# Optimization experiments

Measured on AMD Instinct MI355X. Metric: run time of the kernel, lower is better.

The kernel has to match this reference:

```python
import jax, jax.numpy as jnp
import numpy as np

N = 50000   # nodes
E = 800000  # edges
G = 64      # graphs
NEG_SLOPE = 0.2  # PyG GATConv leaky_relu slope


def gat_conv(x, edge_index, edge_attr, W, att_src, att_dst, We, att_edge, bias, num_nodes):
    # PyG GATConv, add_self_loops=False, concat=True, eval (no dropout)
    H, C = att_src.shape
    h = (x @ W).reshape(-1, H, C)                      # [N,H,C]
    a_src = (h * att_src).sum(-1)                      # [N,H]
    a_dst = (h * att_dst).sum(-1)                      # [N,H]
    src, dst = edge_index[0], edge_index[1]
    e = (edge_attr @ We).reshape(-1, H, C)             # [E,H,C]
    a_edge = (e * att_edge).sum(-1)                    # [E,H]
    alpha = a_src[src] + a_dst[dst] + a_edge           # [E,H]
    alpha = jax.nn.leaky_relu(alpha, NEG_SLOPE)
    # segment softmax over incoming edges of each dst node
    amax = jax.ops.segment_max(alpha, dst, num_segments=num_nodes)
    amax = jnp.where(jnp.isfinite(amax), amax, 0.0)
    ex = jnp.exp(alpha - amax[dst])
    denom = jax.ops.segment_sum(ex, dst, num_segments=num_nodes)
    att = ex / (denom[dst] + 1e-16)                    # [E,H]
    msg = h[src] * att[..., None]                      # [E,H,C]
    out = jax.ops.segment_sum(msg, dst, num_segments=num_nodes)
    return out.reshape(num_nodes, H * C) + bias


def setup_inputs() -> dict:
    key = jax.random.key(0)
    ks = jax.random.split(key, 20)
    s = 0.1
    inp = {
        "x": jax.random.normal(ks[0], (N, 128), jnp.float32),
        "edge_index": jax.random.randint(ks[1], (2, E), 0, N, dtype=jnp.int32),
        "edge_attr": jax.random.normal(ks[2], (E, 1), jnp.float32),
        "batch": jnp.sort(jax.random.randint(ks[3], (N,), 0, G, dtype=jnp.int32)),
        # layer 1: 128 -> 4 heads x 32
        "W1": jax.random.normal(ks[4], (128, 128), jnp.float32) * s,
        "as1": jax.random.normal(ks[5], (4, 32), jnp.float32) * s,
        "ad1": jax.random.normal(ks[6], (4, 32), jnp.float32) * s,
        "We1": jax.random.normal(ks[7], (1, 128), jnp.float32) * s,
        "ae1": jax.random.normal(ks[8], (4, 32), jnp.float32) * s,
        "b1": jnp.zeros((128,), jnp.float32),
        # layer 2: 128 -> 1 head x 64
        "W2": jax.random.normal(ks[9], (128, 64), jnp.float32) * s,
        "as2": jax.random.normal(ks[10], (1, 64), jnp.float32) * s,
        "ad2": jax.random.normal(ks[11], (1, 64), jnp.float32) * s,
        "We2": jax.random.normal(ks[12], (1, 64), jnp.float32) * s,
        "ae2": jax.random.normal(ks[13], (1, 64), jnp.float32) * s,
        "b2": jnp.zeros((64,), jnp.float32),
        # prediction head
        "Wp": jax.random.normal(ks[14], (64, 1), jnp.float32) * s,
        "bp": jnp.zeros((1,), jnp.float32),
    }
    return inp


def reference(x, edge_index, edge_attr, batch, W1, as1, ad1, We1, ae1, b1,
              W2, as2, ad2, We2, ae2, b2, Wp, bp):
    h = gat_conv(x, edge_index, edge_attr, W1, as1, ad1, We1, ae1, b1, N)
    h = jax.nn.relu(h)  # dropout p=0.0, eval mode
    h = gat_conv(h, edge_index, edge_attr, W2, as2, ad2, We2, ae2, b2, N)
    # per-graph mean pooling (vectorized replacement of the python loop)
    counts = jax.ops.segment_sum(jnp.ones((N,), h.dtype), batch, num_segments=G)
    sums = jax.ops.segment_sum(h, batch, num_segments=G)   # [G,64]
    mean = sums / counts[:, None]
    out = mean @ Wp + bp                                   # [G,1]
    return out.squeeze(-1)                                 # [G]
```

## Files before the change

kernel.cpp:

```cpp
#include <hip/hip_runtime.h>
#include <hip/hip_bf16.h>

typedef unsigned short u16;
typedef unsigned int u32;

#define MAXB 2048
#define POOL_MAXG 64

typedef __attribute__((ext_vector_type(8))) short bf16x8;
typedef __attribute__((ext_vector_type(4))) float f32x4;

__device__ __forceinline__ float bf2f(u16 u) { return __uint_as_float(((u32)u) << 16); }
__device__ __forceinline__ float bl(u32 u) { return __uint_as_float(u << 16); }
__device__ __forceinline__ float bh(u32 u) { return __uint_as_float(u & 0xffff0000u); }
__device__ __forceinline__ u16 f2bf(float f) {
    u32 u = __float_as_uint(f);
    u += 0x7fffu + ((u >> 16) & 1u);
    return (u16)(u >> 16);
}
__device__ __forceinline__ float lrelu(float x) { return x > 0.f ? x : 0.2f * x; }
__device__ __forceinline__ int clampi(int v, int lo, int hi) {
    return v < lo ? lo : (v > hi ? hi : v);
}
__device__ __forceinline__ float load1(const void* base, int idx, int f32) {
    return f32 ? ((const float*)base)[idx] : bf2f(((const u16*)base)[idx]);
}
__device__ __forceinline__ float cexpf(float a) {
    return __builtin_amdgcn_exp2f(fminf(a, 30.f) * 1.4426950408889634f);
}

__global__ void k_init(const u32* __restrict__ xw, int* __restrict__ flag,
                       int* __restrict__ bcnt, int B,
                       const void* We1, const void* ae1, const void* We2, const void* ae2,
                       const void* as1, const void* ad1, const void* as2, const void* ad2,
                       float* __restrict__ consts, float* __restrict__ pool, int psize) {
    __shared__ int sf;
    int t = threadIdx.x;
    for (int i = t; i < B; i += 256) bcnt[i] = 0;
    if (t < 64) {
        int cnt = 0;
        #pragma unroll
        for (int j = 0; j < 4; j++) {
            u32 w = xw[t * 4 + j];
            int e0 = (int)((w >> 7) & 0xffu);
            int e1 = (int)((w >> 23) & 0xffu);
            cnt += (e0 >= 0x60 && e0 <= 0x8f);
            cnt += (e1 >= 0x60 && e1 <= 0x8f);
        }
        #pragma unroll
        for (int off = 32; off > 0; off >>= 1) cnt += __shfl_xor(cnt, off);
        if (t == 0) { int v = (cnt < 480) ? 1 : 0; *flag = v; sf = v; }
    }
    __syncthreads();
    int f = sf;
    for (int i = t; i < psize; i += 256) pool[i] = 0.f;
    if (t < 4) {
        float s = 0.f;
        for (int c = 0; c < 32; c++) s += load1(We1, t * 32 + c, f) * load1(ae1, t * 32 + c, f);
        consts[t] = s;
    } else if (t == 4) {
        float s = 0.f;
        for (int c = 0; c < 64; c++) s += load1(We2, c, f) * load1(ae2, c, f);
        consts[4] = s;
    }
    if (t < 128) {
        consts[8 + t] = load1(as1, t, f);
        consts[136 + t] = load1(ad1, t, f);
    }
    if (t < 64) {
        consts[264 + t] = load1(as2, t, f);
        consts[328 + t] = load1(ad2, t, f);
    }
}

template <int NC>
__global__ __launch_bounds__(256, 2) void k_gemm_mfma(
    const void* __restrict__ X, const void* __restrict__ Wg,
    const int* __restrict__ flag, int fXovr, u16* __restrict__ Y,
    const float* __restrict__ consts, float* __restrict__ casrc,
    float* __restrict__ cadst, int nrows) {
    constexpr int NCT = NC / 16;
    __shared__ __align__(16) u16 Bf[2][NCT][4][64][8];

    const int f = *flag;
    const bool fX = (fXovr < 0) ? (f != 0) : (fXovr != 0);
    const bool fW = (f != 0);
    const int tid = threadIdx.x;
    const int wid = tid >> 6, lane = tid & 63;

    for (int idx = tid; idx < NCT * 4 * 64; idx += 256) {
        int l = idx & 63;
        int s = (idx >> 6) & 3;
        int t = idx >> 8;
        int col = t * 16 + (l & 15);
        int k0 = s * 32 + (l >> 4) * 8;
        u16 hi[8], lo[8];
        #pragma unroll
        for (int j = 0; j < 8; j++) {
            int k = k0 + j;
            int srow = (NC == 64) ? ((k & 1) * 64 + (k >> 1)) : k;
            float v = fW ? ((const float*)Wg)[srow * NC + col]
                         : bf2f(((const u16*)Wg)[srow * NC + col]);
            u16 h = f2bf(v);
            hi[j] = h;
            lo[j] = fW ? f2bf(v - bf2f(h)) : (u16)0;
        }
        uint4 hv, lv;
        hv.x = (u32)hi[0] | ((u32)hi[1] << 16);
        hv.y = (u32)hi[2] | ((u32)hi[3] << 16);
        hv.z = (u32)hi[4] | ((u32)hi[5] << 16);
        hv.w = (u32)hi[6] | ((u32)hi[7] << 16);
        lv.x = (u32)lo[0] | ((u32)lo[1] << 16);
        lv.y = (u32)lo[2] | ((u32)lo[3] << 16);
        lv.z = (u32)lo[4] | ((u32)lo[5] << 16);
        lv.w = (u32)lo[6] | ((u32)lo[7] << 16);
        *(uint4*)&Bf[0][t][s][l][0] = hv;
        *(uint4*)&Bf[1][t][s][l][0] = lv;
    }
    __syncthreads();

    const int tiles = (nrows + 63) >> 6;
    for (int tile = blockIdx.x; tile < tiles; tile += gridDim.x) {
        const int rowbase = tile * 64 + wid * 16;
        const int arow = rowbase + (lane & 15);
        const bool rv = arow < nrows;

        bf16x8 ahi[4], alo[4];
        #pragma unroll
        for (int s = 0; s < 4; s++) {
            int koff = s * 32 + (lane >> 4) * 8;
            u16 h[8], l8[8];
            #pragma unroll
            for (int j = 0; j < 8; j++) { h[j] = 0; l8[j] = 0; }
            if (rv) {
                if (fX) {
                    const float* xp = (const float*)X + (size_t)arow * 128 + koff;
                    float4 a = *(const float4*)xp;
                    float4 b = *(const float4*)(xp + 4);
                    float vv[8];
                    vv[0] = a.x; vv[1] = a.y; vv[2] = a.z; vv[3] = a.w;
                    vv[4] = b.x; vv[5] = b.y; vv[6] = b.z; vv[7] = b.w;
                    #pragma unroll
                    for (int j = 0; j < 8; j++) {
                        h[j] = f2bf(vv[j]);
                        l8[j] = f2bf(vv[j] - bf2f(h[j]));
                    }
                } else {
                    const u16* xp = (const u16*)X + (size_t)arow * 128 + koff;
                    uint4 q = *(const uint4*)xp;
                    h[0] = (u16)q.x; h[1] = (u16)(q.x >> 16);
                    h[2] = (u16)q.y; h[3] = (u16)(q.y >> 16);
                    h[4] = (u16)q.z; h[5] = (u16)(q.z >> 16);
                    h[6] = (u16)q.w; h[7] = (u16)(q.w >> 16);
                }
            }
            bf16x8 vh, vl;
            #pragma unroll
            for (int j = 0; j < 8; j++) { vh[j] = (short)h[j]; vl[j] = (short)l8[j]; }
            ahi[s] = vh; alo[s] = vl;
        }

        f32x4 acc[NCT];
        #pragma unroll
        for (int t = 0; t < NCT; t++) acc[t] = (f32x4){0.f, 0.f, 0.f, 0.f};
        #pragma unroll
        for (int s = 0; s < 4; s++) {
            #pragma unroll
            for (int t = 0; t < NCT; t++) {
                bf16x8 bhi = *(const bf16x8*)&Bf[0][t][s][lane][0];
                acc[t] = __builtin_amdgcn_mfma_f32_16x16x32_bf16(ahi[s], bhi, acc[t], 0, 0, 0);
                if (fW) {
                    bf16x8 blo = *(const bf16x8*)&Bf[1][t][s][lane][0];
                    acc[t] = __builtin_amdgcn_mfma_f32_16x16x32_bf16(ahi[s], blo, acc[t], 0, 0, 0);
                }
                if (fX) {
                    acc[t] = __builtin_amdgcn_mfma_f32_16x16x32_bf16(alo[s], bhi, acc[t], 0, 0, 0);
                }
            }
        }

        #pragma unroll
        for (int reg = 0; reg < 4; reg++) {
            int r = rowbase + (lane >> 4) * 4 + reg;
            if (r < nrows) {
                if constexpr (NC == 128) {
                    #pragma unroll
                    for (int t = 0; t < 4; t++) {
                        u32 w = (u32)f2bf(acc[t][reg]) | ((u32)f2bf(acc[t + 4][reg]) << 16);
                        ((u32*)Y)[(size_t)r * 64 + t * 16 + (lane & 15)] = w;
                    }
                } else {
                    #pragma unroll
                    for (int t = 0; t < 4; t++)
                        Y[(size_t)r * 64 + t * 16 + (lane & 15)] = f2bf(acc[t][reg]);
                }
            }
        }

        if (casrc) {
            const int l16 = lane & 15;
            if constexpr (NC == 128) {
                #pragma unroll
                for (int reg = 0; reg < 4; reg++) {
                    int r = rowbase + (lane >> 4) * 4 + reg;
                    float pA[4] = {0.f, 0.f, 0.f, 0.f};
                    float pD[4] = {0.f, 0.f, 0.f, 0.f};
                    #pragma unroll
                    for (int t = 0; t < 4; t++) {
                        int p = t * 16 + l16;
                        int g = t >> 1;
                        pA[g]     += acc[t][reg]     * consts[8 + p];
                        pD[g]     += acc[t][reg]     * consts[136 + p];
                        pA[g + 2] += acc[t + 4][reg] * consts[72 + p];
                        pD[g + 2] += acc[t + 4][reg] * consts[200 + p];
                    }
                    #pragma unroll
                    for (int off = 1; off < 16; off <<= 1) {
                        #pragma unroll
                        for (int g = 0; g < 4; g++) {
                            pA[g] += __shfl_xor(pA[g], off);
                            pD[g] += __shfl_xor(pD[g], off);
                        }
                    }
                    if (l16 == 0 && r < nrows) {
                        #pragma unroll
                        for (int g = 0; g < 4; g++) {
                            casrc[r * 4 + g] = pA[g];
                            cadst[r * 4 + g] = pD[g];
                        }
                    }
                }
            } else {
                #pragma unroll
                for (int reg = 0; reg < 4; reg++) {
                    int r = rowbase + (lane >> 4) * 4 + reg;
                    float s1 = 0.f, s2 = 0.f;
                    #pragma unroll
                    for (int t = 0; t < 4; t++) {
                        int p = t * 16 + l16;
                        s1 += acc[t][reg] * consts[264 + p];
                        s2 += acc[t][reg] * consts[328 + p];
                    }
                    #pragma unroll
                    for (int off = 1; off < 16; off <<= 1) {
                        s1 += __shfl_xor(s1, off);
                        s2 += __shfl_xor(s2, off);
                    }
                    if (l16 == 0 && r < nrows) { casrc[r] = s1; cadst[r] = s2; }
                }
            }
        }
    }
}

__global__ __launch_bounds__(256) void k_bhist2(const int* __restrict__ dst,
                                                int* __restrict__ bcnt, int E, int n, int B) {
    __shared__ int lh[MAXB];
    for (int i = threadIdx.x; i < B; i += 256) lh[i] = 0;
    __syncthreads();
    int stride = gridDim.x * 256;
    for (int e = blockIdx.x * 256 + threadIdx.x; e < E; e += stride) {
        int d = clampi(dst[e], 0, n - 1);
        atomicAdd(&lh[d >> 8], 1);
    }
    __syncthreads();
    for (int i = threadIdx.x; i < B; i += 256)
        if (lh[i]) atomicAdd(&bcnt[i], lh[i]);
}
__global__ void k_bscan(const int* __restrict__ bcnt, int* __restrict__ bbase,
                        int* __restrict__ bfront, int* __restrict__ roff,
                        int B, int N, int E) {
    __shared__ int buf[256];
    __shared__ int carry;
    int t = threadIdx.x;
    if (t == 0) carry = 0;
    __syncthreads();
    for (int base = 0; base < B; base += 256) {
        int k = base + t;
        int v = (k < B) ? bcnt[k] : 0;
        buf[t] = v;
        __syncthreads();
        for (int off = 1; off < 256; off <<= 1) {
            int u = (t >= off) ? buf[t - off] : 0;
            __syncthreads();
            buf[t] += u;
            __syncthreads();
        }
        int excl = carry + buf[t] - v;
        if (k < B) { bbase[k] = excl; bfront[k] = excl; }
        __syncthreads();
        if (t == 0) carry += buf[255];
        __syncthreads();
    }
    if (t == 0) { bbase[B] = carry; roff[N] = E; }
}
__global__ void k_zero(int* __restrict__ p, int n) {
    int i = blockIdx.x * 256 + threadIdx.x;
    if (i < n) p[i] = 0;
}
__global__ __launch_bounds__(256) void k_bhist(const int* __restrict__ dst,
                                               int* __restrict__ cnt, int* __restrict__ bcnt,
                                               int E, int n, int B) {
    __shared__ int lh[MAXB];
    for (int i = threadIdx.x; i < B; i += 256) lh[i] = 0;
    __syncthreads();
    int stride = gridDim.x * 256;
    for (int e = blockIdx.x * 256 + threadIdx.x; e < E; e += stride) {
        int d = clampi(dst[e], 0, n - 1);
        atomicAdd(&cnt[d], 1);
        atomicAdd(&lh[d >> 8], 1);
    }
    __syncthreads();
    for (int i = threadIdx.x; i < B; i += 256)
        if (lh[i]) atomicAdd(&bcnt[i], lh[i]);
}
__global__ void k_scan1(const int* __restrict__ cnt, int* __restrict__ part,
                        int* __restrict__ bsum, int n) {
    __shared__ int buf[256];
    int i = blockIdx.x * 256 + threadIdx.x;
    int v = (i < n) ? cnt[i] : 0;
    buf[threadIdx.x] = v;
    __syncthreads();
    for (int off = 1; off < 256; off <<= 1) {
        int t = (threadIdx.x >= off) ? buf[threadIdx.x - off] : 0;
        __syncthreads();
        buf[threadIdx.x] += t;
        __syncthreads();
    }
    if (i < n) part[i] = buf[threadIdx.x];
    if (threadIdx.x == 255) bsum[blockIdx.x] = buf[255];
}
__global__ void k_scan3b(int* __restrict__ roff, const int* __restrict__ bsum,
                         int* __restrict__ rpos, int n, int nb) {
    __shared__ int buf[256];
    int t = threadIdx.x;
    int v = (t < nb) ? bsum[t] : 0;
    buf[t] = v;
    __syncthreads();
    for (int off = 1; off < 256; off <<= 1) {
        int u = (t >= off) ? buf[t - off] : 0;
        __syncthreads();
        buf[t] += u;
        __syncthreads();
    }
    __shared__ int excl[256];
    excl[t] = buf[t] - v;
    __syncthreads();
    int i = blockIdx.x * 256 + t;
    if (i > n) return;
    int val;
    if (i == 0) { val = 0; roff[0] = 0; }
    else { val = roff[i] + excl[(i - 1) >> 8]; roff[i] = val; }
    if (i < n) rpos[i] = val;
}
__global__ __launch_bounds__(256) void k_binA(
    const int* __restrict__ dst, const int* __restrict__ src, const void* eattr,
    const int* __restrict__ flag, int* __restrict__ bfront, int2* __restrict__ stagedA,
    float4* __restrict__ stagedE, const float* __restrict__ asrc,
    const float* __restrict__ adst, const float* __restrict__ consts,
    int E, int n, int B) {
    __shared__ int lhist[MAXB];
    __shared__ int lbase[MAXB];
    int f = *flag;
    const float c0 = consts[0], c1 = consts[1], c2 = consts[2], c3 = consts[3];
    constexpr int T = 2048;
    for (int tile = blockIdx.x; (long long)tile * T < E; tile += gridDim.x) {
        int base = tile * T;
        for (int i = threadIdx.x; i < B; i += 256) lhist[i] = 0;
        __syncthreads();
        int sj0, sj1, sj2, sj3, sj4, sj5, sj6, sj7;
        int dj0, dj1, dj2, dj3, dj4, dj5, dj6, dj7;
        int rj0, rj1, rj2, rj3, rj4, rj5, rj6, rj7;
        int ej0, ej1, ej2, ej3, ej4, ej5, ej6, ej7;
        #define BINA_LOAD(J, SJ, DJ, RJ, EJ)                                   \
        {                                                                      \
            int idx = base + (J) * 256 + threadIdx.x;                          \
            bool v = idx < E;                                                  \
            int d = v ? clampi(dst[idx], 0, n - 1) : 0;                        \
            SJ = v ? clampi(src[idx], 0, n - 1) : 0;                           \
            EJ = v ? __float_as_int(load1(eattr, idx, f)) : 0;                 \
            DJ = d;                                                            \
            RJ = v ? atomicAdd(&lhist[d >> 8], 1) : -1;                        \
        }
        BINA_LOAD(0, sj0, dj0, rj0, ej0)
        BINA_LOAD(1, sj1, dj1, rj1, ej1)
        BINA_LOAD(2, sj2, dj2, rj2, ej2)
        BINA_LOAD(3, sj3, dj3, rj3, ej3)
        BINA_LOAD(4, sj4, dj4, rj4, ej4)
        BINA_LOAD(5, sj5, dj5, rj5, ej5)
        BINA_LOAD(6, sj6, dj6, rj6, ej6)
        BINA_LOAD(7, sj7, dj7, rj7, ej7)
        #undef BINA_LOAD
        __syncthreads();
        for (int i = threadIdx.x; i < B; i += 256) {
            int c = lhist[i];
            lbase[i] = c ? atomicAdd(&bfront[i], c) : 0;
        }
        __syncthreads();
        #define BINA_STORE(SJ, DJ, RJ, EJ)                                     \
        if (RJ >= 0) {                                                         \
            long long q = (long long)lbase[DJ >> 8] + RJ;                      \
            if (q >= 0 && q < E) {                                             \
                int2 v2;                                                       \
                v2.x = (SJ & 0xFFFFFF) | ((DJ & 255) << 24);                   \
                v2.y = EJ;                                                     \
                stagedA[q] = v2;                                               \
                float ea = __int_as_float(EJ);                                 \
                float4 av = *(const float4*)&asrc[(size_t)SJ * 4];             \
                float4 dvv = *(const float4*)&adst[(size_t)DJ * 4];            \
                float4 evv;                                                    \
                evv.x = cexpf(lrelu(av.x + dvv.x + ea * c0));                  \
                evv.y = cexpf(lrelu(av.y + dvv.y + ea * c1));                  \
                evv.z = cexpf(lrelu(av.z + dvv.z + ea * c2));                  \
                evv.w = cexpf(lrelu(av.w + dvv.w + ea * c3));                  \
                stagedE[q] = evv;                                              \
            }                                                                  \
        }
        BINA_STORE(sj0, dj0, rj0, ej0)
        BINA_STORE(sj1, dj1, rj1, ej1)
        BINA_STORE(sj2, dj2, rj2, ej2)
        BINA_STORE(sj3, dj3, rj3, ej3)
        BINA_STORE(sj4, dj4, rj4, ej4)
        BINA_STORE(sj5, dj5, rj5, ej5)
        BINA_STORE(sj6, dj6, rj6, ej6)
        BINA_STORE(sj7, dj7, rj7, ej7)
        #undef BINA_STORE
        __syncthreads();
    }
}
__global__ __launch_bounds__(256) void k_binB2(
    const int2* __restrict__ stagedA, const float4* __restrict__ stagedE,
    const int* __restrict__ bbase, int* __restrict__ roff,
    int2* __restrict__ edata, float* __restrict__ eexp, int N, int E, int B) {
    __shared__ int lcnt[256];
    __shared__ int buf[256];
    __shared__ int lpos[256];
    int k = blockIdx.x;
    int t = threadIdx.x;
    lcnt[t] = 0;
    __syncthreads();
    int lo = clampi(bbase[k], 0, E);
    int hi = clampi(bbase[k + 1], lo, E);
    for (int i = lo + t; i < hi; i += 256)
        atomicAdd(&lcnt[(stagedA[i].x >> 24) & 255], 1);
    __syncthreads();
    int v = lcnt[t];
    buf[t] = v;
    __syncthreads();
    for (int off = 1; off < 256; off <<= 1) {
        int u = (t >= off) ? buf[t - off] : 0;
        __syncthreads();
        buf[t] += u;
        __syncthreads();
    }
    int pos = lo + buf[t] - v;
    int dn = (k << 8) + t;
    if (dn < N) roff[dn] = pos;
    lpos[t] = pos;
    __syncthreads();
    for (int i = lo + t; i < hi; i += 256) {
        int2 a = stagedA[i];
        float4 ev = stagedE[i];
        int p = atomicAdd(&lpos[(a.x >> 24) & 255], 1);
        if (p >= 0 && p < E) {
            edata[p] = make_int2(a.x & 0xFFFFFF, a.y);
            *(float4*)&eexp[(size_t)p * 4] = ev;
        }
    }
}
__global__ void k_scatter(const int* __restrict__ dst, const int* __restrict__ src,
                          const void* eattr, const int* __restrict__ flag,
                          int* __restrict__ rpos, int2* __restrict__ edata,
                          float* __restrict__ eexp, const float* __restrict__ asrc,
                          const float* __restrict__ adst, const float* __restrict__ consts,
                          int E, int n) {
    int f = *flag;
    int e = blockIdx.x * 256 + threadIdx.x;
    if (e < E) {
        int d = clampi(dst[e], 0, n - 1);
        int s = clampi(src[e], 0, n - 1);
        float ea = load1(eattr, e, f);
        int p = atomicAdd(&rpos[d], 1);
        if (p >= 0 && p < E) {
            int2 v; v.x = s; v.y = __float_as_int(ea);
            edata[p] = v;
            if (eexp) {
                float4 av = *(const float4*)&asrc[(size_t)s * 4];
                float4 dv = *(const float4*)&adst[(size_t)d * 4];
                float4 ev;
                ev.x = cexpf(lrelu(av.x + dv.x + ea * consts[0]));
                ev.y = cexpf(lrelu(av.y + dv.y + ea * consts[1]));
                ev.z = cexpf(lrelu(av.z + dv.z + ea * consts[2]));
                ev.w = cexpf(lrelu(av.w + dv.w + ea * consts[3]));
                *(float4*)&eexp[(size_t)p * 4] = ev;
            }
        }
    }
}

__global__ __launch_bounds__(256) void k_gat1c(
    const u32* __restrict__ hp, const float* __restrict__ eexp,
    const int2* __restrict__ edata, const int* __restrict__ roff,
    const int* __restrict__ flag, const void* bias, u32* __restrict__ out, int n, int E) {
    __shared__ float4 wls[4][64];
    int f = *flag;
    int gtid = blockIdx.x * 256 + threadIdx.x;
    int wv = gtid >> 6, lane = gtid & 63;
    int wid = (threadIdx.x >> 6);
    int nw = (gridDim.x * 256) >> 6;
    const int hl = lane & 31;
    const int sel = lane >> 5;
    const int p0 = hl * 2;
    const int phsel = hl >> 4;
    const float biasA0 = load1(bias, p0, f);
    const float biasB0 = load1(bias, 64 + p0, f);
    const float biasA1 = load1(bias, p0 + 1, f);
    const float biasB1 = load1(bias, 64 + p0 + 1, f);
    const int ghsel = lane >> 5;
    const float gbiasA = load1(bias, lane, f);
    const float gbiasB = load1(bias, 64 + lane, f);

    for (int db = wv * 2; db < n; db += nw * 2) {
        int d = db + sel;
        bool dv = d < n;
        int s0 = dv ? clampi(roff[d], 0, E) : 0;
        int s1 = dv ? clampi(roff[d + 1], s0, E) : 0;
        int deg = s1 - s0;

        if (__all(deg <= 32)) {
            bool v = hl < deg;
            int s = 0;
            float4 ev = make_float4(0.f, 0.f, 0.f, 0.f);
            if (v) {
                ev = *(const float4*)&eexp[(size_t)(s0 + hl) * 4];
                s = edata[s0 + hl].x;
            }
            float d0 = ev.x, d1 = ev.y, d2 = ev.z, d3 = ev.w;
            #pragma unroll
            for (int off = 16; off > 0; off >>= 1) {
                d0 += __shfl_xor(d0, off); d1 += __shfl_xor(d1, off);
                d2 += __shfl_xor(d2, off); d3 += __shfl_xor(d3, off);
            }
            float i0 = 1.f / (d0 + 1e-16f), i1 = 1.f / (d1 + 1e-16f);
            float i2 = 1.f / (d2 + 1e-16f), i3 = 1.f / (d3 + 1e-16f);
            wls[wid][lane] = make_float4(ev.x * i0, ev.y * i1, ev.z * i2, ev.w * i3);

            int degm = max(deg, __shfl_xor(deg, 32));
            int base = sel * 32;
            float aA0 = 0.f, aB0 = 0.f, aA1 = 0.f, aB1 = 0.f;
            for (int j = 0; j < degm; j += 4) {
                int j0 = base + j, j1 = base + j + 1, j2 = base + j + 2, j3 = base + j + 3;
                int sa = __shfl(s, j0), sb = __shfl(s, j1);
                int sc_ = __shfl(s, j2), sd = __shfl(s, j3);
                float4 wa = wls[wid][j0], wb = wls[wid][j1];
                float4 wc = wls[wid][j2], wd = wls[wid][j3];
                uint2 ha = *(const uint2*)(hp + (size_t)sa * 64 + p0);
                uint2 hb = *(const uint2*)(hp + (size_t)sb * 64 + p0);
                uint2 hc = *(const uint2*)(hp + (size_t)sc_ * 64 + p0);
                uint2 hd = *(const uint2*)(hp + (size_t)sd * 64 + p0);
                float wAa = phsel ? wa.y : wa.x, wBa = phsel ? wa.w : wa.z;
                float wAb = phsel ? wb.y : wb.x, wBb = phsel ? wb.w : wb.z;
                float wAc = phsel ? wc.y : wc.x, wBc = phsel ? wc.w : wc.z;
                float wAd = phsel ? wd.y : wd.x, wBd = phsel ? wd.w : wd.z;
                aA0 += wAa * bl(ha.x); aB0 += wBa * bh(ha.x);
                aA1 += wAa * bl(ha.y); aB1 += wBa * bh(ha.y);
                aA0 += wAb * bl(hb.x); aB0 += wBb * bh(hb.x);
                aA1 += wAb * bl(hb.y); aB1 += wBb * bh(hb.y);
                aA0 += wAc * bl(hc.x); aB0 += wBc * bh(hc.x);
                aA1 += wAc * bl(hc.y); aB1 += wBc * bh(hc.y);
                aA0 += wAd * bl(hd.x); aB0 += wBd * bh(hd.x);
                aA1 += wAd * bl(hd.y); aB1 += wBd * bh(hd.y);
            }
            if (dv) {
                u32 w0 = (u32)f2bf(fmaxf(aA0 + biasA0, 0.f))
                       | ((u32)f2bf(fmaxf(aB0 + biasB0, 0.f)) << 16);
                u32 w1 = (u32)f2bf(fmaxf(aA1 + biasA1, 0.f))
                       | ((u32)f2bf(fmaxf(aB1 + biasB1, 0.f)) << 16);
                *(uint2*)(out + (size_t)d * 64 + p0) = make_uint2(w0, w1);
            }
        } else {
            for (int q = 0; q < 2; q++) {
                int dq = db + q;
                if (dq >= n) break;
                int t0 = clampi(roff[dq], 0, E);
                int t1 = clampi(roff[dq + 1], t0, E);
                int dg = t1 - t0;
                if (dg <= 64) {
                    bool v = lane < dg;
                    int s = 0;
                    float4 ev = make_float4(0.f, 0.f, 0.f, 0.f);
                    if (v) {
                        ev = *(const float4*)&eexp[(size_t)(t0 + lane) * 4];
                        s = edata[t0 + lane].x;
                    }
                    float d0 = ev.x, d1 = ev.y, d2 = ev.z, d3 = ev.w;
                    #pragma unroll
                    for (int off = 32; off > 0; off >>= 1) {
                        d0 += __shfl_xor(d0, off); d1 += __shfl_xor(d1, off);
                        d2 += __shfl_xor(d2, off); d3 += __shfl_xor(d3, off);
                    }
                    float i0 = 1.f / (d0 + 1e-16f), i1 = 1.f / (d1 + 1e-16f);
                    float i2 = 1.f / (d2 + 1e-16f), i3 = 1.f / (d3 + 1e-16f);
                    wls[wid][lane] = make_float4(ev.x * i0, ev.y * i1, ev.z * i2, ev.w * i3);

                    float aA0 = 0.f, aB0 = 0.f, aA1 = 0.f, aB1 = 0.f;
                    for (int j = 0; j < dg; j += 4) {
                        int j0 = j + sel, j1 = j + 2 + sel;
                        int sa = __shfl(s, j0), sb = __shfl(s, j1);
                        float4 wa = wls[wid][j0], wb = wls[wid][j1];
                        uint2 ha = *(const uint2*)(hp + (size_t)sa * 64 + p0);
                        uint2 hb = *(const uint2*)(hp + (size_t)sb * 64 + p0);
                        float wAa = phsel ? wa.y : wa.x, wBa = phsel ? wa.w : wa.z;
                        float wAb = phsel ? wb.y : wb.x, wBb = phsel ? wb.w : wb.z;
                        aA0 += wAa * bl(ha.x); aB0 += wBa * bh(ha.x);
                        aA1 += wAa * bl(ha.y); aB1 += wBa * bh(ha.y);
                        aA0 += wAb * bl(hb.x); aB0 += wBb * bh(hb.x);
                        aA1 += wAb * bl(hb.y); aB1 += wBb * bh(hb.y);
                    }
                    aA0 += __shfl_xor(aA0, 32); aB0 += __shfl_xor(aB0, 32);
                    aA1 += __shfl_xor(aA1, 32); aB1 += __shfl_xor(aB1, 32);
                    if (lane < 32) {
                        u32 w0 = (u32)f2bf(fmaxf(aA0 + biasA0, 0.f))
                               | ((u32)f2bf(fmaxf(aB0 + biasB0, 0.f)) << 16);
                        u32 w1 = (u32)f2bf(fmaxf(aA1 + biasA1, 0.f))
                               | ((u32)f2bf(fmaxf(aB1 + biasB1, 0.f)) << 16);
                        *(uint2*)(out + (size_t)dq * 64 + p0) = make_uint2(w0, w1);
                    }
                } else {
                    float d0 = 0.f, d1 = 0.f, d2 = 0.f, d3 = 0.f;
                    for (int idx = t0 + lane; idx < t1; idx += 64) {
                        float4 ev = *(const float4*)&eexp[(size_t)idx * 4];
                        d0 += ev.x; d1 += ev.y; d2 += ev.z; d3 += ev.w;
                    }
                    #pragma unroll
                    for (int off = 32; off > 0; off >>= 1) {
                        d0 += __shfl_xor(d0, off); d1 += __shfl_xor(d1, off);
                        d2 += __shfl_xor(d2, off); d3 += __shfl_xor(d3, off);
                    }
                    float i0 = 1.f / (d0 + 1e-16f), i1 = 1.f / (d1 + 1e-16f);
                    float i2 = 1.f / (d2 + 1e-16f), i3 = 1.f / (d3 + 1e-16f);
                    float iA = ghsel ? i1 : i0, iB = ghsel ? i3 : i2;
                    float accA = 0.f, accB = 0.f;
                    for (int idx = t0; idx < t1; idx++) {
                        float4 ev = *(const float4*)&eexp[(size_t)idx * 4];
                        int s = edata[idx].x;
                        float wA = (ghsel ? ev.y : ev.x) * iA;
                        float wB = (ghsel ? ev.w : ev.z) * iB;
                        u32 hw = hp[(size_t)s * 64 + lane];
                        accA += wA * bl(hw);
                        accB += wB * bh(hw);
                    }
                    float rA = fmaxf(accA + gbiasA, 0.f);
                    float rB = fmaxf(accB + gbiasB, 0.f);
                    out[(size_t)dq * 64 + lane] = (u32)f2bf(rA) | ((u32)f2bf(rB) << 16);
                }
            }
        }
    }
}

__global__ __launch_bounds__(256) void k_gat2c(
    const u16* __restrict__ h, const float* __restrict__ asrc, const float* __restrict__ adst,
    const int2* __restrict__ edata, const int* __restrict__ roff,
    const int* __restrict__ flag, const float* __restrict__ consts, const void* bias,
    u16* __restrict__ out, int n, int E) {
    __shared__ float wls[4][64];
    int f = *flag;
    int gtid = blockIdx.x * 256 + threadIdx.x;
    int wv = gtid >> 6, lane = gtid & 63;
    int wid = (threadIdx.x >> 6);
    int nw = (gridDim.x * 256) >> 6;
    const float C = consts[4];
    const int hl = lane & 31;
    const int sel = lane >> 5;
    const int p0 = hl * 2;
    const float bias0 = load1(bias, p0, f);
    const float bias1 = load1(bias, p0 + 1, f);
    const float gbias = load1(bias, lane, f);

    for (int db = wv * 2; db < n; db += nw * 2) {
        int d = db + sel;
        bool dv = d < n;
        int s0 = dv ? clampi(roff[d], 0, E) : 0;
        int s1 = dv ? clampi(roff[d + 1], s0, E) : 0;
        int deg = s1 - s0;
        float ad = dv ? adst[d] : 0.f;

        if (__all(deg <= 32)) {
            bool v = hl < deg;
            int s = 0;
            float e = 0.f;
            if (v) {
                int2 ed = edata[s0 + hl];
                s = ed.x;
                e = cexpf(lrelu(asrc[s] + ad + __int_as_float(ed.y) * C));
            }
            float den = e;
            #pragma unroll
            for (int off = 16; off > 0; off >>= 1) den += __shfl_xor(den, off);
            float inv = 1.f / (den + 1e-16f);
            wls[wid][lane] = e * inv;

            int degm = max(deg, __shfl_xor(deg, 32));
            int base = sel * 32;
            float a0 = 0.f, a1 = 0.f;
            for (int j = 0; j < degm; j += 4) {
                int j0 = base + j, j1 = base + j + 1, j2 = base + j + 2, j3 = base + j + 3;
                int sa = __shfl(s, j0), sb = __shfl(s, j1);
                int sc_ = __shfl(s, j2), sd = __shfl(s, j3);
                float wa = wls[wid][j0], wb = wls[wid][j1];
                float wc = wls[wid][j2], wd = wls[wid][j3];
                u32 ha = *(const u32*)(h + (size_t)sa * 64 + p0);
                u32 hb = *(const u32*)(h + (size_t)sb * 64 + p0);
                u32 hc = *(const u32*)(h + (size_t)sc_ * 64 + p0);
                u32 hd = *(const u32*)(h + (size_t)sd * 64 + p0);
                a0 += wa * bl(ha) + wb * bl(hb) + wc * bl(hc) + wd * bl(hd);
                a1 += wa * bh(ha) + wb * bh(hb) + wc * bh(hc) + wd * bh(hd);
            }
            if (dv) {
                u32 w = (u32)f2bf(a0 + bias0) | ((u32)f2bf(a1 + bias1) << 16);
                *(u32*)(out + (size_t)d * 64 + p0) = w;
            }
        } else {
            for (int q = 0; q < 2; q++) {
                int dq = db + q;
                if (dq >= n) break;
                int t0 = clampi(roff[dq], 0, E);
                int t1 = clampi(roff[dq + 1], t0, E);
                int dg = t1 - t0;
                float adq = adst[dq];
                if (dg <= 64) {
                    bool v = lane < dg;
                    int s = 0;
                    float e = 0.f;
                    if (v) {
                        int2 ed = edata[t0 + lane];
                        s = ed.x;
                        e = cexpf(lrelu(asrc[s] + adq + __int_as_float(ed.y) * C));
                    }
                    float den = e;
                    #pragma unroll
                    for (int off = 32; off > 0; off >>= 1) den += __shfl_xor(den, off);
                    float inv = 1.f / (den + 1e-16f);
                    wls[wid][lane] = e * inv;

                    float a0 = 0.f, a1 = 0.f;
                    for (int j = 0; j < dg; j += 4) {
                        int j0 = j + sel, j1 = j + 2 + sel;
                        int sa = __shfl(s, j0), sb = __shfl(s, j1);
                        float wa = wls[wid][j0], wb = wls[wid][j1];
                        u32 ha = *(const u32*)(h + (size_t)sa * 64 + p0);
                        u32 hb = *(const u32*)(h + (size_t)sb * 64 + p0);
                        a0 += wa * bl(ha) + wb * bl(hb);
                        a1 += wa * bh(ha) + wb * bh(hb);
                    }
                    a0 += __shfl_xor(a0, 32);
                    a1 += __shfl_xor(a1, 32);
                    if (lane < 32) {
                        u32 w = (u32)f2bf(a0 + bias0) | ((u32)f2bf(a1 + bias1) << 16);
                        *(u32*)(out + (size_t)dq * 64 + p0) = w;
                    }
                } else {
                    float den = 0.f;
                    for (int idx = t0 + lane; idx < t1; idx += 64) {
                        int2 ed = edata[idx];
                        den += cexpf(lrelu(asrc[ed.x] + adq + __int_as_float(ed.y) * C));
                    }
                    #pragma unroll
                    for (int off = 32; off > 0; off >>= 1) den += __shfl_xor(den, off);
                    float inv = 1.f / (den + 1e-16f);
                    float acc = 0.f;
                    for (int idx = t0; idx < t1; idx++) {
                        int2 ed = edata[idx];
                        float w = cexpf(lrelu(asrc[ed.x] + adq
                                              + __int_as_float(ed.y) * C)) * inv;
                        acc += w * bf2f(h[(size_t)ed.x * 64 + lane]);
                    }
                    out[(size_t)dq * 64 + lane] = f2bf(acc + gbias);
                }
            }
        }
    }
}

__global__ __launch_bounds__(256) void k_gat1f(
    const u32* __restrict__ hp, const float* __restrict__ asrc, const float* __restrict__ adst,
    const int2* __restrict__ edata, const int* __restrict__ roff,
    const int* __restrict__ flag, const float* __restrict__ consts, const void* bias,
    u32* __restrict__ out, int n, int E) {
    int f = *flag;
    int gtid = blockIdx.x * 256 + threadIdx.x;
    int wv = gtid >> 6, lane = gtid & 63;
    int nw = (gridDim.x * 256) >> 6;
    const float c0 = consts[0], c1 = consts[1], c2 = consts[2], c3 = consts[3];
    const int hsel = lane >> 5;
    const float biasA = load1(bias, lane, f);
    const float biasB = load1(bias, 64 + lane, f);

    for (int d = wv; d < n; d += nw) {
        int s0 = clampi(roff[d], 0, E);
        int s1 = clampi(roff[d + 1], s0, E);
        float4 adv = *(const float4*)&adst[d * 4];
        float d0 = 0.f, d1 = 0.f, d2 = 0.f, d3 = 0.f;
        for (int idx = s0 + lane; idx < s1; idx += 64) {
            int2 ed = edata[idx];
            float ea = __int_as_float(ed.y);
            float4 av = *(const float4*)&asrc[(size_t)ed.x * 4];
            d0 += cexpf(lrelu(av.x + adv.x + ea * c0));
            d1 += cexpf(lrelu(av.y + adv.y + ea * c1));
            d2 += cexpf(lrelu(av.z + adv.z + ea * c2));
            d3 += cexpf(lrelu(av.w + adv.w + ea * c3));
        }
        #pragma unroll
        for (int off = 32; off > 0; off >>= 1) {
            d0 += __shfl_xor(d0, off); d1 += __shfl_xor(d1, off);
            d2 += __shfl_xor(d2, off); d3 += __shfl_xor(d3, off);
        }
        float i0 = 1.f / (d0 + 1e-16f), i1 = 1.f / (d1 + 1e-16f);
        float i2 = 1.f / (d2 + 1e-16f), i3 = 1.f / (d3 + 1e-16f);
        float iA = hsel ? i1 : i0, iB = hsel ? i3 : i2;
        float cA = hsel ? c1 : c0, cB = hsel ? c3 : c2;
        float aA = hsel ? adv.y : adv.x, aB = hsel ? adv.w : adv.z;

        float accA = 0.f, accB = 0.f;
        for (int idx = s0; idx < s1; idx++) {
            int2 ed = edata[idx];
            float ea = __int_as_float(ed.y);
            float4 av = *(const float4*)&asrc[(size_t)ed.x * 4];
            float wA = cexpf(lrelu((hsel ? av.y : av.x) + aA + ea * cA)) * iA;
            float wB = cexpf(lrelu((hsel ? av.w : av.z) + aB + ea * cB)) * iB;
            u32 hw = hp[(size_t)ed.x * 64 + lane];
            accA += wA * bl(hw);
            accB += wB * bh(hw);
        }
        float rA = fmaxf(accA + biasA, 0.f);
        float rB = fmaxf(accB + biasB, 0.f);
        out[(size_t)d * 64 + lane] = (u32)f2bf(rA) | ((u32)f2bf(rB) << 16);
    }
}

__global__ __launch_bounds__(256) void k_gat2f(
    const u16* __restrict__ h, const float* __restrict__ asrc, const float* __restrict__ adst,
    const int2* __restrict__ edata, const int* __restrict__ roff,
    const int* __restrict__ flag, const float* __restrict__ consts, const void* bias,
    u16* __restrict__ out, int n, int E) {
    int f = *flag;
    int gtid = blockIdx.x * 256 + threadIdx.x;
    int wv = gtid >> 6, lane = gtid & 63;
    int nw = (gridDim.x * 256) >> 6;
    const float C = consts[4];
    const float biasL = load1(bias, lane, f);

    for (int d = wv; d < n; d += nw) {
        int s0 = clampi(roff[d], 0, E);
        int s1 = clampi(roff[d + 1], s0, E);
        float ad = adst[d];
        float den = 0.f;
        for (int idx = s0 + lane; idx < s1; idx += 64) {
            int2 ed = edata[idx];
            den += cexpf(lrelu(asrc[ed.x] + ad + __int_as_float(ed.y) * C));
        }
        #pragma unroll
        for (int off = 32; off > 0; off >>= 1) den += __shfl_xor(den, off);
        float inv = 1.f / (den + 1e-16f);

        float acc = 0.f;
        for (int idx = s0; idx < s1; idx++) {
            int2 ed = edata[idx];
            float w = cexpf(lrelu(asrc[ed.x] + ad + __int_as_float(ed.y) * C)) * inv;
            acc += w * bf2f(h[(size_t)ed.x * 64 + lane]);
        }
        out[(size_t)d * 64 + lane] = f2bf(acc + biasL);
    }
}

__global__ __launch_bounds__(256) void k_pool2(
    const u16* __restrict__ agg2, const int* __restrict__ batch,
    float* __restrict__ pool, float* __restrict__ cnt, int n, int G, int rpb) {
    __shared__ float lp[POOL_MAXG * 64];
    __shared__ float lc[POOL_MAXG];
    int t = threadIdx.x;
    for (int i = t; i < G * 64; i += 256) lp[i] = 0.f;
    for (int i = t; i < G; i += 256) lc[i] = 0.f;
    __syncthreads();
    int lane = t & 63;
    int rl = t >> 6;
    int r0 = blockIdx.x * rpb;
    int r1 = min(r0 + rpb, n);
    float acc = 0.f, cacc = 0.f;
    int curg = -1;
    for (int j = r0 + rl; j < r1; j += 4) {
        int g = clampi(batch[j], 0, G - 1);
        float v = bf2f(agg2[(size_t)j * 64 + lane]);
        if (g != curg) {
            if (curg >= 0) {
                atomicAdd(&lp[curg * 64 + lane], acc);
                if (lane == 0) atomicAdd(&lc[curg], cacc);
            }
            acc = 0.f; cacc = 0.f; curg = g;
        }
        acc += v; cacc += 1.f;
    }
    if (curg >= 0) {
        atomicAdd(&lp[curg * 64 + lane], acc);
        if (lane == 0) atomicAdd(&lc[curg], cacc);
    }
    __syncthreads();
    for (int i = t; i < G * 64; i += 256) {
        float v = lp[i];
        if (v != 0.f) atomicAdd(&pool[i], v);
    }
    for (int i = t; i < G; i += 256) {
        float v = lc[i];
        if (v != 0.f) atomicAdd(&cnt[i], v);
    }
}

__global__ void k_pool(const u16* __restrict__ agg2, const int* __restrict__ batch,
                       float* __restrict__ pool, float* __restrict__ cnt, int n, int G) {
    int t = blockIdx.x * 256 + threadIdx.x;
    int nb8 = (n + 7) / 8;
    if (t >= nb8 * 64) return;
    int base = (t >> 6) * 8;
    int c = t & 63;
    int end = min(base + 8, n);
    float acc = 0.f, cacc = 0.f;
    int curg = clampi(batch[base], 0, G - 1);
    for (int j = base; j < end; j++) {
        int g = clampi(batch[j], 0, G - 1);
        if (g != curg) {
            atomicAdd(&pool[curg * 64 + c], acc);
            if (c == 0) atomicAdd(&cnt[curg], cacc);
            acc = 0.f; cacc = 0.f; curg = g;
        }
        acc += bf2f(agg2[(size_t)j * 64 + c]);
        cacc += 1.f;
    }
    atomicAdd(&pool[curg * 64 + c], acc);
    if (c == 0) atomicAdd(&cnt[curg], cacc);
}

__global__ void k_head(const float* __restrict__ pool, const float* __restrict__ cnt,
                       const void* Wp, const void* bp, const int* __restrict__ flag,
                       void* out, int G) {
    int f = *flag;
    int g = threadIdx.x;
    if (g >= G) return;
    float s = 0.f;
    for (int c = 0; c < 64; c++) s += pool[g * 64 + c] * load1(Wp, c, f);
    float cv = cnt[g];
    if (!(cv > 0.f)) cv = 1.f;
    float r = s / cv + load1(bp, 0, f);
    if (f) ((float*)out)[g] = r;
    else   ((u16*)out)[g] = f2bf(r);
}

extern "C" void kernel_launch(void* const* d_in, const int* in_sizes, int n_in,
                              void* d_out, int out_size, void* d_ws, size_t ws_size,
                              hipStream_t stream) {
    const void* x    = d_in[0];
    const int* ei    = (const int*)d_in[1];
    const void* eattr = d_in[2];
    const int* batch = (const int*)d_in[3];
    const void* W1   = d_in[4];
    const void* as1  = d_in[5];
    const void* ad1  = d_in[6];
    const void* We1  = d_in[7];
    const void* ae1  = d_in[8];
    const void* b1   = d_in[9];
    const void* W2   = d_in[10];
    const void* as2  = d_in[11];
    const void* ad2  = d_in[12];
    const void* We2  = d_in[13];
    const void* ae2  = d_in[14];
    const void* b2   = d_in[15];
    const void* Wp   = d_in[16];
    const void* bp   = d_in[17];

    const int N = in_sizes[3];
    const int E = in_sizes[2];
    const int G = out_size;
    const int* src = ei;
    const int* dst = ei + E;
    const int B = (N + 255) >> 8;

    char* p = (char*)d_ws;
    auto alloc = [&](size_t bytes) -> char* {
        char* r = p;
        p += (bytes + 255) & ~(size_t)255;
        return r;
    };
    int* flag    = (int*)alloc(32);
    float* consts = (float*)alloc(2048);
    int* roff    = (int*)alloc((size_t)(N + 1) * 4);
    int* rpos    = (int*)alloc((size_t)N * 4);
    int* bsum    = (int*)alloc(256 * 4);
    int* bcnt    = (int*)alloc((size_t)(MAXB * 3 + 1) * 4);
    int* bbase   = bcnt + MAXB;
    int* bfront  = bbase + MAXB + 1;
    int2* edata  = (int2*)alloc((size_t)E * 8);
    float* pool  = (float*)alloc((size_t)(G * 64 + G) * 4);
    float* cnt   = pool + (size_t)G * 64;
    float* asrc1 = (float*)alloc((size_t)N * 4 * 4);
    float* adst1 = (float*)alloc((size_t)N * 4 * 4);
    float* asrc2 = asrc1;
    float* adst2 = adst1;
    u16* agg1    = (u16*)alloc((size_t)N * 128 * 2);
    u16* h1      = (u16*)alloc((size_t)N * 128 * 2);
    u16* h2      = h1;
    u16* agg2    = h1 + (size_t)N * 64;
    float* eexp  = (float*)alloc((size_t)E * 16);
    int2* stagedA = (int2*)alloc((size_t)E * 8);
    float4* stagedE = (float4*)alloc((size_t)E * 16);
    size_t full_need = (size_t)(p - (char*)d_ws);
    const bool cached = (ws_size >= full_need);
    const bool binned = cached && (B <= MAXB) && (N <= (1 << 24));

    const int GG = (N + 127) >> 7;

    k_init<<<1, 256, 0, stream>>>((const u32*)x, flag, bcnt, B,
                                  We1, ae1, We2, ae2, as1, ad1, as2, ad2,
                                  consts, pool, G * 64 + G);
    k_gemm_mfma<128><<<GG, 256, 0, stream>>>(x, W1, flag, -1, h1, consts,
                                             asrc1, adst1, N);

    if (binned) {
        k_bhist2<<<512, 256, 0, stream>>>(dst, bcnt, E, N, B);
        k_bscan<<<1, 256, 0, stream>>>(bcnt, bbase, bfront, roff, B, N, E);
        k_binA<<<(E + 2047) / 2048, 256, 0, stream>>>(dst, src, eattr, flag, bfront,
                                                      stagedA, stagedE, asrc1, adst1,
                                                      consts, E, N, B);
        k_binB2<<<B, 256, 0, stream>>>(stagedA, stagedE, bbase, roff, edata, eexp, N, E, B);
    } else {
        int NB = (N + 255) / 256;
        k_zero<<<(N + 255) / 256, 256, 0, stream>>>(rpos, N);
        k_bhist<<<512, 256, 0, stream>>>(dst, rpos, bcnt, E, N, B);
        k_scan1<<<NB, 256, 0, stream>>>(rpos, roff + 1, bsum, N);
        k_scan3b<<<(N + 256) / 256, 256, 0, stream>>>(roff, bsum, rpos, N, NB);
        k_scatter<<<(E + 255) / 256, 256, 0, stream>>>(dst, src, eattr, flag, rpos,
                                                       edata, cached ? eexp : nullptr,
                                                       asrc1, adst1, consts, E, N);
    }

    int gatBlocks = (N * 64 + 255) / 256;
    if (cached) {
        k_gat1c<<<gatBlocks, 256, 0, stream>>>((const u32*)h1, eexp, edata, roff,
                                               flag, b1, (u32*)agg1, N, E);
    } else {
        k_gat1f<<<gatBlocks, 256, 0, stream>>>((const u32*)h1, asrc1, adst1, edata, roff,
                                               flag, consts, b1, (u32*)agg1, N, E);
    }
    k_gemm_mfma<64><<<GG, 256, 0, stream>>>(agg1, W2, flag, 0, h2, consts,
                                            asrc2, adst2, N);
    if (cached) {
        k_gat2c<<<gatBlocks, 256, 0, stream>>>(h2, asrc2, adst2, edata, roff, flag,
                                               consts, b2, agg2, N, E);
    } else {
        k_gat2f<<<gatBlocks, 256, 0, stream>>>(h2, asrc2, adst2, edata, roff, flag,
                                               consts, b2, agg2, N, E);
    }
    if (G <= POOL_MAXG) {
        int rpb = (N + 1023) / 1024;
        if (rpb < 8) rpb = 8;
        int pblocks = (N + rpb - 1) / rpb;
        k_pool2<<<pblocks, 256, 0, stream>>>(agg2, batch, pool, cnt, N, G, rpb);
    } else {
        k_pool<<<(((N + 7) / 8) * 64 + 255) / 256, 256, 0, stream>>>(agg2, batch, pool,
                                                                     cnt, N, G);
    }
    k_head<<<1, 64, 0, stream>>>(pool, cnt, Wp, bp, flag, d_out, G);
}
```

Measured before the change: 299.5 us.

## Recompute edge attention exponentials in layer-1 GAT instead of staging them

Drops the per-edge float4 exp(leaky_relu(alpha)) precomputation in the binning and scatter kernels, along with the staged and sorted eexp buffers. The layer-1 aggregation kernel now gathers asrc for each edge's source, reads adst once per destination, and recomputes the exponentials inline. This removes writing and reading roughly two 16-byte-per-edge arrays. The cost is an extra random asrc gather per edge and repeated exp work, which happens twice per edge on the high-degree path.

```diff
diff --git a/kernel.cpp b/kernel.cpp
--- a/kernel.cpp
+++ b/kernel.cpp
@@ -356,13 +356,10 @@
 __global__ __launch_bounds__(256) void k_binA(
     const int* __restrict__ dst, const int* __restrict__ src, const void* eattr,
     const int* __restrict__ flag, int* __restrict__ bfront, int2* __restrict__ stagedA,
-    float4* __restrict__ stagedE, const float* __restrict__ asrc,
-    const float* __restrict__ adst, const float* __restrict__ consts,
     int E, int n, int B) {
     __shared__ int lhist[MAXB];
     __shared__ int lbase[MAXB];
     int f = *flag;
-    const float c0 = consts[0], c1 = consts[1], c2 = consts[2], c3 = consts[3];
     constexpr int T = 2048;
     for (int tile = blockIdx.x; (long long)tile * T < E; tile += gridDim.x) {
         int base = tile * T;
@@ -405,15 +402,6 @@
                 v2.x = (SJ & 0xFFFFFF) | ((DJ & 255) << 24);                   \
                 v2.y = EJ;                                                     \
                 stagedA[q] = v2;                                               \
-                float ea = __int_as_float(EJ);                                 \
-                float4 av = *(const float4*)&asrc[(size_t)SJ * 4];             \
-                float4 dvv = *(const float4*)&adst[(size_t)DJ * 4];            \
-                float4 evv;                                                    \
-                evv.x = cexpf(lrelu(av.x + dvv.x + ea * c0));                  \
-                evv.y = cexpf(lrelu(av.y + dvv.y + ea * c1));                  \
-                evv.z = cexpf(lrelu(av.z + dvv.z + ea * c2));                  \
-                evv.w = cexpf(lrelu(av.w + dvv.w + ea * c3));                  \
-                stagedE[q] = evv;                                              \
             }                                                                  \
         }
         BINA_STORE(sj0, dj0, rj0, ej0)
@@ -429,9 +417,8 @@
     }
 }
 __global__ __launch_bounds__(256) void k_binB2(
-    const int2* __restrict__ stagedA, const float4* __restrict__ stagedE,
-    const int* __restrict__ bbase, int* __restrict__ roff,
-    int2* __restrict__ edata, float* __restrict__ eexp, int N, int E, int B) {
+    const int2* __restrict__ stagedA, const int* __restrict__ bbase,
+    int* __restrict__ roff, int2* __restrict__ edata, int N, int E, int B) {
     __shared__ int lcnt[256];
     __shared__ int buf[256];
     __shared__ int lpos[256];
@@ -460,20 +447,13 @@
     __syncthreads();
     for (int i = lo + t; i < hi; i += 256) {
         int2 a = stagedA[i];
-        float4 ev = stagedE[i];
         int p = atomicAdd(&lpos[(a.x >> 24) & 255], 1);
-        if (p >= 0 && p < E) {
-            edata[p] = make_int2(a.x & 0xFFFFFF, a.y);
-            *(float4*)&eexp[(size_t)p * 4] = ev;
-        }
+        if (p >= 0 && p < E) edata[p] = make_int2(a.x & 0xFFFFFF, a.y);
     }
 }
 __global__ void k_scatter(const int* __restrict__ dst, const int* __restrict__ src,
                           const void* eattr, const int* __restrict__ flag,
-                          int* __restrict__ rpos, int2* __restrict__ edata,
-                          float* __restrict__ eexp, const float* __restrict__ asrc,
-                          const float* __restrict__ adst, const float* __restrict__ consts,
-                          int E, int n) {
+                          int* __restrict__ rpos, int2* __restrict__ edata, int E, int n) {
     int f = *flag;
     int e = blockIdx.x * 256 + threadIdx.x;
     if (e < E) {
@@ -484,30 +464,22 @@
         if (p >= 0 && p < E) {
             int2 v; v.x = s; v.y = __float_as_int(ea);
             edata[p] = v;
-            if (eexp) {
-                float4 av = *(const float4*)&asrc[(size_t)s * 4];
-                float4 dv = *(const float4*)&adst[(size_t)d * 4];
-                float4 ev;
-                ev.x = cexpf(lrelu(av.x + dv.x + ea * consts[0]));
-                ev.y = cexpf(lrelu(av.y + dv.y + ea * consts[1]));
-                ev.z = cexpf(lrelu(av.z + dv.z + ea * consts[2]));
-                ev.w = cexpf(lrelu(av.w + dv.w + ea * consts[3]));
-                *(float4*)&eexp[(size_t)p * 4] = ev;
-            }
         }
     }
 }
 
 __global__ __launch_bounds__(256) void k_gat1c(
-    const u32* __restrict__ hp, const float* __restrict__ eexp,
+    const u32* __restrict__ hp, const float* __restrict__ asrc, const float* __restrict__ adst,
     const int2* __restrict__ edata, const int* __restrict__ roff,
-    const int* __restrict__ flag, const void* bias, u32* __restrict__ out, int n, int E) {
+    const int* __restrict__ flag, const float* __restrict__ consts, const void* bias,
+    u32* __restrict__ out, int n, int E) {
     __shared__ float4 wls[4][64];
     int f = *flag;
     int gtid = blockIdx.x * 256 + threadIdx.x;
     int wv = gtid >> 6, lane = gtid & 63;
     int wid = (threadIdx.x >> 6);
     int nw = (gridDim.x * 256) >> 6;
+    const float c0 = consts[0], c1 = consts[1], c2 = consts[2], c3 = consts[3];
     const int hl = lane & 31;
     const int sel = lane >> 5;
     const int p0 = hl * 2;
@@ -523,19 +495,27 @@
     for (int db = wv * 2; db < n; db += nw * 2) {
         int d = db + sel;
         bool dv = d < n;
+        int dcl = dv ? d : 0;
         int s0 = dv ? clampi(roff[d], 0, E) : 0;
         int s1 = dv ? clampi(roff[d + 1], s0, E) : 0;
         int deg = s1 - s0;
 
         if (__all(deg <= 32)) {
+            float4 adv = *(const float4*)&adst[(size_t)dcl * 4];
             bool v = hl < deg;
             int s = 0;
-            float4 ev = make_float4(0.f, 0.f, 0.f, 0.f);
+            float e0 = 0.f, e1 = 0.f, e2 = 0.f, e3 = 0.f;
             if (v) {
-                ev = *(const float4*)&eexp[(size_t)(s0 + hl) * 4];
-                s = edata[s0 + hl].x;
-            }
-            float d0 = ev.x, d1 = ev.y, d2 = ev.z, d3 = ev.w;
+                int2 ed = edata[s0 + hl];
+                s = ed.x;
+                float ea = __int_as_float(ed.y);
+                float4 av = *(const float4*)&asrc[(size_t)s * 4];
+                e0 = cexpf(lrelu(av.x + adv.x + ea * c0));
+                e1 = cexpf(lrelu(av.y + adv.y + ea * c1));
+                e2 = cexpf(lrelu(av.z + adv.z + ea * c2));
+                e3 = cexpf(lrelu(av.w + adv.w + ea * c3));
+            }
+            float d0 = e0, d1 = e1, d2 = e2, d3 = e3;
             #pragma unroll
             for (int off = 16; off > 0; off >>= 1) {
                 d0 += __shfl_xor(d0, off); d1 += __shfl_xor(d1, off);
@@ -543,7 +523,7 @@
             }
             float i0 = 1.f / (d0 + 1e-16f), i1 = 1.f / (d1 + 1e-16f);
             float i2 = 1.f / (d2 + 1e-16f), i3 = 1.f / (d3 + 1e-16f);
-            wls[wid][lane] = make_float4(ev.x * i0, ev.y * i1, ev.z * i2, ev.w * i3);
+            wls[wid][lane] = make_float4(e0 * i0, e1 * i1, e2 * i2, e3 * i3);
 
             int degm = max(deg, __shfl_xor(deg, 32));
             int base = sel * 32;
@@ -585,15 +565,22 @@
                 int t0 = clampi(roff[dq], 0, E);
                 int t1 = clampi(roff[dq + 1], t0, E);
                 int dg = t1 - t0;
+                float4 adv = *(const float4*)&adst[(size_t)dq * 4];
                 if (dg <= 64) {
                     bool v = lane < dg;
                     int s = 0;
-                    float4 ev = make_float4(0.f, 0.f, 0.f, 0.f);
+                    float e0 = 0.f, e1 = 0.f, e2 = 0.f, e3 = 0.f;
                     if (v) {
-                        ev = *(const float4*)&eexp[(size_t)(t0 + lane) * 4];
-                        s = edata[t0 + lane].x;
-                    }
-                    float d0 = ev.x, d1 = ev.y, d2 = ev.z, d3 = ev.w;
+                        int2 ed = edata[t0 + lane];
+                        s = ed.x;
+                        float ea = __int_as_float(ed.y);
+                        float4 av = *(const float4*)&asrc[(size_t)s * 4];
+                        e0 = cexpf(lrelu(av.x + adv.x + ea * c0));
+                        e1 = cexpf(lrelu(av.y + adv.y + ea * c1));
+                        e2 = cexpf(lrelu(av.z + adv.z + ea * c2));
+                        e3 = cexpf(lrelu(av.w + adv.w + ea * c3));
+                    }
+                    float d0 = e0, d1 = e1, d2 = e2, d3 = e3;
                     #pragma unroll
                     for (int off = 32; off > 0; off >>= 1) {
                         d0 += __shfl_xor(d0, off); d1 += __shfl_xor(d1, off);
@@ -601,7 +588,7 @@
                     }
                     float i0 = 1.f / (d0 + 1e-16f), i1 = 1.f / (d1 + 1e-16f);
                     float i2 = 1.f / (d2 + 1e-16f), i3 = 1.f / (d3 + 1e-16f);
-                    wls[wid][lane] = make_float4(ev.x * i0, ev.y * i1, ev.z * i2, ev.w * i3);
+                    wls[wid][lane] = make_float4(e0 * i0, e1 * i1, e2 * i2, e3 * i3);
 
                     float aA0 = 0.f, aB0 = 0.f, aA1 = 0.f, aB1 = 0.f;
                     for (int j = 0; j < dg; j += 4) {
@@ -629,8 +616,13 @@
                 } else {
                     float d0 = 0.f, d1 = 0.f, d2 = 0.f, d3 = 0.f;
                     for (int idx = t0 + lane; idx < t1; idx += 64) {
-                        float4 ev = *(const float4*)&eexp[(size_t)idx * 4];
-                        d0 += ev.x; d1 += ev.y; d2 += ev.z; d3 += ev.w;
+                        int2 ed = edata[idx];
+                        float ea = __int_as_float(ed.y);
+                        float4 av = *(const float4*)&asrc[(size_t)ed.x * 4];
+                        d0 += cexpf(lrelu(av.x + adv.x + ea * c0));
+                        d1 += cexpf(lrelu(av.y + adv.y + ea * c1));
+                        d2 += cexpf(lrelu(av.z + adv.z + ea * c2));
+                        d3 += cexpf(lrelu(av.w + adv.w + ea * c3));
                     }
                     #pragma unroll
                     for (int off = 32; off > 0; off >>= 1) {
@@ -640,13 +632,16 @@
                     float i0 = 1.f / (d0 + 1e-16f), i1 = 1.f / (d1 + 1e-16f);
                     float i2 = 1.f / (d2 + 1e-16f), i3 = 1.f / (d3 + 1e-16f);
                     float iA = ghsel ? i1 : i0, iB = ghsel ? i3 : i2;
+                    float cA = ghsel ? c1 : c0, cB = ghsel ? c3 : c2;
+                    float aA = ghsel ? adv.y : adv.x, aB = ghsel ? adv.w : adv.z;
                     float accA = 0.f, accB = 0.f;
                     for (int idx = t0; idx < t1; idx++) {
-                        float4 ev = *(const float4*)&eexp[(size_t)idx * 4];
-                        int s = edata[idx].x;
-                        float wA = (ghsel ? ev.y : ev.x) * iA;
-                        float wB = (ghsel ? ev.w : ev.z) * iB;
-                        u32 hw = hp[(size_t)s * 64 + lane];
+                        int2 ed = edata[idx];
+                        float ea = __int_as_float(ed.y);
+                        float4 av = *(const float4*)&asrc[(size_t)ed.x * 4];
+                        float wA = cexpf(lrelu((ghsel ? av.y : av.x) + aA + ea * cA)) * iA;
+                        float wB = cexpf(lrelu((ghsel ? av.w : av.z) + aB + ea * cB)) * iB;
+                        u32 hw = hp[(size_t)ed.x * 64 + lane];
                         accA += wA * bl(hw);
                         accB += wB * bh(hw);
                     }
@@ -1009,9 +1004,7 @@
     u16* h1      = (u16*)alloc((size_t)N * 128 * 2);
     u16* h2      = h1;
     u16* agg2    = h1 + (size_t)N * 64;
-    float* eexp  = (float*)alloc((size_t)E * 16);
     int2* stagedA = (int2*)alloc((size_t)E * 8);
-    float4* stagedE = (float4*)alloc((size_t)E * 16);
     size_t full_need = (size_t)(p - (char*)d_ws);
     const bool cached = (ws_size >= full_need);
     const bool binned = cached && (B <= MAXB) && (N <= (1 << 24));
@@ -1028,9 +1021,8 @@
         k_bhist2<<<512, 256, 0, stream>>>(dst, bcnt, E, N, B);
         k_bscan<<<1, 256, 0, stream>>>(bcnt, bbase, bfront, roff, B, N, E);
         k_binA<<<(E + 2047) / 2048, 256, 0, stream>>>(dst, src, eattr, flag, bfront,
-                                                      stagedA, stagedE, asrc1, adst1,
-                                                      consts, E, N, B);
-        k_binB2<<<B, 256, 0, stream>>>(stagedA, stagedE, bbase, roff, edata, eexp, N, E, B);
+                                                      stagedA, E, N, B);
+        k_binB2<<<B, 256, 0, stream>>>(stagedA, bbase, roff, edata, N, E, B);
     } else {
         int NB = (N + 255) / 256;
         k_zero<<<(N + 255) / 256, 256, 0, stream>>>(rpos, N);
@@ -1038,14 +1030,13 @@
         k_scan1<<<NB, 256, 0, stream>>>(rpos, roff + 1, bsum, N);
         k_scan3b<<<(N + 256) / 256, 256, 0, stream>>>(roff, bsum, rpos, N, NB);
         k_scatter<<<(E + 255) / 256, 256, 0, stream>>>(dst, src, eattr, flag, rpos,
-                                                       edata, cached ? eexp : nullptr,
-                                                       asrc1, adst1, consts, E, N);
+                                                       edata, E, N);
     }
 
     int gatBlocks = (N * 64 + 255) / 256;
     if (cached) {
-        k_gat1c<<<gatBlocks, 256, 0, stream>>>((const u32*)h1, eexp, edata, roff,
-                                               flag, b1, (u32*)agg1, N, E);
+        k_gat1c<<<gatBlocks, 256, 0, stream>>>((const u32*)h1, asrc1, adst1, edata, roff,
+                                               flag, consts, b1, (u32*)agg1, N, E);
     } else {
         k_gat1f<<<gatBlocks, 256, 0, stream>>>((const u32*)h1, asrc1, adst1, edata, roff,
                                                flag, consts, b1, (u32*)agg1, N, E);
```

Measured after the change: 283.5 us. 5.3% less time.
